# Kernel tuning notes

Measured on AMD Instinct MI355X. Metric: run time of the kernel, lower is better.

## Reference

```python
import jax, jax.numpy as jnp
import numpy as np

N_LAYERS = 4
BN_EPS = 1e-5


def setup_inputs() -> dict:
    key = jax.random.key(0)
    ks = jax.random.split(key, 10)
    N, E, F, H = 50000, 600000, 128, 128
    x = jax.random.normal(ks[0], (N, F), dtype=jnp.float32)
    edge_index = jax.random.randint(ks[1], (2, E), 0, N, dtype=jnp.int64)
    s = 0.05  # small init to keep deep ReLU stack numerically tame
    return {
        "x": x,
        "edge_index": edge_index,
        # stacked params for the 4 GINConv MLPs (num_features == hidden)
        "conv_w1": jax.random.normal(ks[2], (N_LAYERS, F, H), dtype=jnp.float32) * s,
        "conv_b1": jnp.zeros((N_LAYERS, H), dtype=jnp.float32),
        "conv_gamma": jnp.ones((N_LAYERS, H), dtype=jnp.float32),
        "conv_beta": jnp.zeros((N_LAYERS, H), dtype=jnp.float32),
        "conv_w2": jax.random.normal(ks[3], (N_LAYERS, H, H), dtype=jnp.float32) * s,
        "conv_b2": jnp.zeros((N_LAYERS, H), dtype=jnp.float32),
        "fc1_w": jax.random.normal(ks[4], (H, H), dtype=jnp.float32) * s,
        "fc1_b": jnp.zeros((H,), dtype=jnp.float32),
        "fc2_w": jax.random.normal(ks[5], (H, 1), dtype=jnp.float32) * s,
        "fc2_b": jnp.zeros((1,), dtype=jnp.float32),
    }


def _batchnorm(h, gamma, beta):
    # training-mode BatchNorm1d: batch stats over the node axis, biased variance
    mean = jnp.mean(h, axis=0, keepdims=True)
    var = jnp.mean(jnp.square(h - mean), axis=0, keepdims=True)
    return (h - mean) * jax.lax.rsqrt(var + BN_EPS) * gamma + beta


def _gin_layer(x, src, dst, w1, b1, gamma, beta, w2, b2):
    n = x.shape[0]
    # GIN sum aggregation with eps=0: (1+eps)*x_i + sum_{j->i} x_j
    agg = x + jax.ops.segment_sum(x[src], dst, num_segments=n)
    h = jax.nn.relu(agg @ w1 + b1)
    h = _batchnorm(h, gamma, beta)
    return jax.nn.relu(h @ w2 + b2)


def reference(x, edge_index, conv_w1, conv_b1, conv_gamma, conv_beta,
              conv_w2, conv_b2, fc1_w, fc1_b, fc2_w, fc2_b):
    src, dst = edge_index[0], edge_index[1]
    h = x
    for l in range(N_LAYERS):
        h = _gin_layer(h, src, dst, conv_w1[l], conv_b1[l], conv_gamma[l],
                       conv_beta[l], conv_w2[l], conv_b2[l])
    h = jax.nn.relu(h @ fc1_w + fc1_b)
    return h @ fc2_w + fc2_b  # [N, 1]
```

## Files before the change

kernel.cpp:

```cpp
#include <hip/hip_runtime.h>

constexpr int FEAT = 128;

typedef __attribute__((ext_vector_type(8))) _Float16 f16x8;
typedef __attribute__((ext_vector_type(4))) float f32x4;

__device__ inline unsigned int halfpair(float a, float b) {
  unsigned short ua = __builtin_bit_cast(unsigned short, (_Float16)a);
  unsigned short ub = __builtin_bit_cast(unsigned short, (_Float16)b);
  return (unsigned int)ua | ((unsigned int)ub << 16);
}
__device__ inline unsigned short halfr(float a) {
  return __builtin_bit_cast(unsigned short, (_Float16)a);
}
__device__ inline float2 halfup(unsigned int u) {
  _Float16 lo = __builtin_bit_cast(_Float16, (unsigned short)(u & 0xffffu));
  _Float16 hi = __builtin_bit_cast(_Float16, (unsigned short)(u >> 16));
  return make_float2((float)lo, (float)hi);
}

__device__ __host__ inline int kperm(int k) {
  return ((k >> 5) << 5) + (((k >> 2) & 3) << 3) + (((k >> 4) & 1) << 2) + (k & 3);
}


__global__ void count_kernel(const int* __restrict__ dst, int* __restrict__ deg, int E) {
  int e = blockIdx.x * blockDim.x + threadIdx.x;
  if (e < E) atomicAdd(&deg[dst[e]], 1);
}

__global__ __launch_bounds__(1024) void scan_kernel(const int* __restrict__ in,
                                                    int* __restrict__ out,
                                                    int* __restrict__ out2, int n) {
  __shared__ int wsum[16];
  __shared__ int carry;
  int tid = threadIdx.x;
  if (tid == 0) carry = 0;
  __syncthreads();
  int lane = tid & 63, wid = tid >> 6;
  for (int base = 0; base < n; base += 1024) {
    int i = base + tid;
    int v = (i < n) ? in[i] : 0;
    int s = v;
#pragma unroll
    for (int off = 1; off < 64; off <<= 1) {
      int t = __shfl_up(s, off);
      if (lane >= off) s += t;
    }
    if (lane == 63) wsum[wid] = s;
    __syncthreads();
    if (tid < 16) {
      int ws2 = wsum[tid];
#pragma unroll
      for (int off = 1; off < 16; off <<= 1) {
        int t = __shfl_up(ws2, off, 16);
        if ((tid & 15) >= off) ws2 += t;
      }
      wsum[tid] = ws2;
    }
    __syncthreads();
    int excl = carry + (wid ? wsum[wid - 1] : 0) + (s - v);
    if (i < n) { out[i] = excl; out2[i] = excl; }
    __syncthreads();
    if (tid == 0) carry += wsum[15];
    __syncthreads();
  }
}

__global__ void fill_kernel(const int* __restrict__ src, const int* __restrict__ dst,
                            int* __restrict__ cursor, int* __restrict__ col, int E) {
  int e = blockIdx.x * blockDim.x + threadIdx.x;
  if (e < E) {
    int p = atomicAdd(&cursor[dst[e]], 1);
    col[p] = src[e];
  }
}


__global__ void convert_kernel(const float* __restrict__ x, unsigned short* __restrict__ xb,
                               int n4) {
  int idx = blockIdx.x * blockDim.x + threadIdx.x;
  if (idx >= n4) return;
  float4 v = ((const float4*)x)[idx];
  uint2 o;
  o.x = halfpair(v.x, v.y);
  o.y = halfpair(v.z, v.w);
  ((uint2*)xb)[idx] = o;
}


__global__ void wconv_kernel(const float* __restrict__ w1, const float* __restrict__ fc1w,
                             unsigned short* __restrict__ dst) {
  int idx = blockIdx.x * blockDim.x + threadIdx.x;
  if (idx >= 5 * FEAT * FEAT) return;
  int m = idx >> 14;
  int r = idx & (FEAT * FEAT - 1);
  int k = r >> 7, n = r & 127;
  float v = (m < 4) ? w1[idx] : fc1w[r];
  int p = kperm(k);
  int slot = p >> 3, e = p & 7;
  dst[m * FEAT * FEAT + n * FEAT + ((slot ^ (n & 7)) << 3) + e] = halfr(v);
}


__global__ void agg_kernel(const unsigned short* __restrict__ x, const int* __restrict__ rowptr,
                           const int* __restrict__ col, unsigned short* __restrict__ agg, int N) {
  int gid = blockIdx.x * blockDim.x + threadIdx.x;
  int wid = gid >> 6;
  int lane = threadIdx.x & 63;
  int node = wid * 4 + (lane >> 4);
  if (node >= N) return;
  int ln = lane & 15;
  const uint4* xr = (const uint4*)x;
  uint4 s = xr[(size_t)node * 16 + ln];
  float2 t0 = halfup(s.x), t1 = halfup(s.y), t2 = halfup(s.z), t3 = halfup(s.w);
  float a0 = t0.x, a1 = t0.y, a2 = t1.x, a3 = t1.y;
  float a4 = t2.x, a5 = t2.y, a6 = t3.x, a7 = t3.y;
  float b0 = 0.f, b1 = 0.f, b2 = 0.f, b3 = 0.f;
  float b4 = 0.f, b5 = 0.f, b6 = 0.f, b7 = 0.f;
  int e0 = rowptr[node], e1 = rowptr[node + 1];
  int e = e0;
  for (; e + 1 < e1; e += 2) {
    int c0 = col[e], c1 = col[e + 1];
    uint4 v = xr[(size_t)c0 * 16 + ln];
    uint4 u = xr[(size_t)c1 * 16 + ln];
    float2 v0 = halfup(v.x), v1 = halfup(v.y), v2 = halfup(v.z), v3 = halfup(v.w);
    float2 u0 = halfup(u.x), u1 = halfup(u.y), u2 = halfup(u.z), u3 = halfup(u.w);
    a0 += v0.x; a1 += v0.y; a2 += v1.x; a3 += v1.y;
    a4 += v2.x; a5 += v2.y; a6 += v3.x; a7 += v3.y;
    b0 += u0.x; b1 += u0.y; b2 += u1.x; b3 += u1.y;
    b4 += u2.x; b5 += u2.y; b6 += u3.x; b7 += u3.y;
  }
  if (e < e1) {
    uint4 v = xr[(size_t)col[e] * 16 + ln];
    float2 v0 = halfup(v.x), v1 = halfup(v.y), v2 = halfup(v.z), v3 = halfup(v.w);
    a0 += v0.x; a1 += v0.y; a2 += v1.x; a3 += v1.y;
    a4 += v2.x; a5 += v2.y; a6 += v3.x; a7 += v3.y;
  }
  a0 += b0; a1 += b1; a2 += b2; a3 += b3;
  a4 += b4; a5 += b5; a6 += b6; a7 += b7;
  uint4 o;
  o.x = halfpair(a0, a1);
  o.y = halfpair(a2, a3);
  o.z = halfpair(a4, a5);
  o.w = halfpair(a6, a7);
  ((uint4*)agg)[(size_t)node * 16 + ln] = o;
}


__global__ __launch_bounds__(256) void gemm_kernel(
    const unsigned short* __restrict__ A, const unsigned short* __restrict__ Wimg,
    const float* __restrict__ bias, unsigned short* __restrict__ C,
    float* __restrict__ pS, float* __restrict__ pQ, int N, int doStats) {
  __shared__ unsigned short Al[FEAT * FEAT];
  __shared__ unsigned short Wl[FEAT * FEAT];
  __shared__ float ls[FEAT], lq[FEAT];

  int tx = threadIdx.x;
  int row0 = blockIdx.x * FEAT;
  if (tx < FEAT) { ls[tx] = 0.f; lq[tx] = 0.f; }

#pragma unroll
  for (int i = 0; i < 8; i++) {
    int idx = tx + i * 256;
    ((uint4*)Wl)[idx] = ((const uint4*)Wimg)[idx];
  }
#pragma unroll
  for (int i = 0; i < 16; i++) {
    int idx = tx + i * 256;
    int r = idx >> 5;
    int c = idx & 31;
    uint2 v = make_uint2(0u, 0u);
    if (row0 + r < N) v = ((const uint2*)(A + (size_t)(row0 + r) * FEAT))[c];
    int k0 = c << 2;
    int p0 = ((k0 >> 5) << 5) + (((k0 >> 2) & 3) << 3) + (((k0 >> 4) & 1) << 2);
    int slot = p0 >> 3, half4 = (p0 >> 2) & 1;
    *(uint2*)&Al[r * FEAT + ((slot ^ (r & 7)) << 3) + (half4 << 2)] = v;
  }
  __syncthreads();

  int w = tx >> 6;
  int l = tx & 63;
  int llo = l & 15, lhi = l >> 4;
  int wr = (w >> 1) * 64, wc = (w & 1) * 64;

  f32x4 acc[4][4];
#pragma unroll
  for (int mi = 0; mi < 4; mi++)
#pragma unroll
    for (int nj = 0; nj < 4; nj++) acc[mi][nj] = (f32x4)(0.f);

#pragma unroll
  for (int s = 0; s < 4; s++) {
    f16x8 af[4], wf[4];
#pragma unroll
    for (int mi = 0; mi < 4; mi++) {
      int row = wr + mi * 16 + llo;
      int base = row * FEAT + ((((s << 2) + lhi) ^ (row & 7)) << 3);
      af[mi] = *(const f16x8*)&Al[base];
    }
#pragma unroll
    for (int nj = 0; nj < 4; nj++) {
      int n = wc + nj * 16 + llo;
      int base = n * FEAT + ((((s << 2) + lhi) ^ (n & 7)) << 3);
      wf[nj] = *(const f16x8*)&Wl[base];
    }
#pragma unroll
    for (int mi = 0; mi < 4; mi++)
#pragma unroll
      for (int nj = 0; nj < 4; nj++)
        acc[mi][nj] = __builtin_amdgcn_mfma_f32_16x16x32_f16(wf[nj], af[mi], acc[mi][nj], 0, 0, 0);
  }

#pragma unroll
  for (int nj = 0; nj < 4; nj++) {
    int colb = wc + nj * 16 + lhi * 4;
    float4 bb = *(const float4*)&bias[colb];
    float ps[4] = {0.f, 0.f, 0.f, 0.f}, pq[4] = {0.f, 0.f, 0.f, 0.f};
#pragma unroll
    for (int mi = 0; mi < 4; mi++) {
      int row = row0 + wr + mi * 16 + llo;
      f32x4 v = acc[mi][nj];
      float v0 = fmaxf(v[0] + bb.x, 0.f);
      float v1 = fmaxf(v[1] + bb.y, 0.f);
      float v2 = fmaxf(v[2] + bb.z, 0.f);
      float v3 = fmaxf(v[3] + bb.w, 0.f);
      if (row < N) {
        *(uint2*)&C[(size_t)row * FEAT + colb] = make_uint2(halfpair(v0, v1), halfpair(v2, v3));
        ps[0] += v0; ps[1] += v1; ps[2] += v2; ps[3] += v3;
        pq[0] += v0 * v0; pq[1] += v1 * v1; pq[2] += v2 * v2; pq[3] += v3 * v3;
      }
    }
    if (doStats) {
#pragma unroll
      for (int r = 0; r < 4; r++) {
        float s2 = ps[r], q2 = pq[r];
#pragma unroll
        for (int off = 1; off < 16; off <<= 1) {
          s2 += __shfl_xor(s2, off);
          q2 += __shfl_xor(q2, off);
        }
        if (llo == 0) {
          atomicAdd(&ls[colb + r], s2);
          atomicAdd(&lq[colb + r], q2);
        }
      }
    }
  }
  if (doStats) {
    __syncthreads();
    if (tx < FEAT) {
      pS[(size_t)blockIdx.x * FEAT + tx] = ls[tx];
      pQ[(size_t)blockIdx.x * FEAT + tx] = lq[tx];
    }
  }
}


__global__ __launch_bounds__(64) void stats_kernel(
    const float* __restrict__ pS, const float* __restrict__ pQ, int nblk,
    const float* __restrict__ gamma, const float* __restrict__ beta,
    float* __restrict__ scf, float* __restrict__ shf, int N) {
  int c = blockIdx.x;
  int ln = threadIdx.x;
  float s = 0.f, q = 0.f;
  for (int b = ln; b < nblk; b += 64) {
    s += pS[(size_t)b * FEAT + c];
    q += pQ[(size_t)b * FEAT + c];
  }
#pragma unroll
  for (int off = 32; off; off >>= 1) {
    s += __shfl_xor(s, off);
    q += __shfl_xor(q, off);
  }
  if (ln == 0) {
    float invN = 1.0f / (float)N;
    float mean = s * invN;
    float var = q * invN - mean * mean;
    float rstd = rsqrtf(var + 1e-5f);
    float scale = gamma[c] * rstd;
    scf[c] = scale;
    shf[c] = beta[c] - mean * scale;
  }
}


__global__ __launch_bounds__(128) void fold2_kernel(
    const float* __restrict__ scf, const float* __restrict__ shf,
    const float* __restrict__ w2, const float* __restrict__ b2,
    unsigned short* __restrict__ w2f, float* __restrict__ b2f) {
  __shared__ float red[FEAT];
  int c = blockIdx.x;
  int k = threadIdx.x;
  float wv = w2[k * FEAT + c];
  int p = kperm(k);
  int slot = p >> 3, e = p & 7;
  w2f[c * FEAT + ((slot ^ (c & 7)) << 3) + e] = halfr(scf[k] * wv);
  red[k] = shf[k] * wv;
  __syncthreads();
#pragma unroll
  for (int off = 64; off > 0; off >>= 1) {
    if (k < off) red[k] += red[k + off];
    __syncthreads();
  }
  if (k == 0) b2f[c] = b2[c] + red[0];
}


__global__ void fc2_kernel(const unsigned short* __restrict__ h, const float* __restrict__ w,
                           const float* __restrict__ b, float* __restrict__ out, int N) {
  int gid = blockIdx.x * blockDim.x + threadIdx.x;
  int node = gid >> 6;
  if (node >= N) return;
  int lane = threadIdx.x & 63;
  float2 hv = halfup(((const unsigned int*)h)[(size_t)node * 64 + lane]);
  float2 wv = ((const float2*)w)[lane];
  float s = hv.x * wv.x + hv.y * wv.y;
#pragma unroll
  for (int off = 32; off; off >>= 1) s += __shfl_xor(s, off);
  if (lane == 0) out[node] = s + b[0];
}


extern "C" void kernel_launch(void* const* d_in, const int* in_sizes, int n_in,
                              void* d_out, int out_size, void* d_ws, size_t ws_size,
                              hipStream_t stream) {
  const float* x     = (const float*)d_in[0];
  const int*   ei    = (const int*)d_in[1];
  const float* w1    = (const float*)d_in[2];
  const float* b1    = (const float*)d_in[3];
  const float* gamma = (const float*)d_in[4];
  const float* beta  = (const float*)d_in[5];
  const float* w2    = (const float*)d_in[6];
  const float* b2    = (const float*)d_in[7];
  const float* fc1w  = (const float*)d_in[8];
  const float* fc1b  = (const float*)d_in[9];
  const float* fc2w  = (const float*)d_in[10];
  const float* fc2b  = (const float*)d_in[11];
  float* out = (float*)d_out;

  int N = in_sizes[0] / FEAT;
  int E = in_sizes[1] / 2;
  const int* srcI = ei;
  const int* dstI = ei + E;

  int gemmBlocks = (N + FEAT - 1) / FEAT;

  size_t Nf = (size_t)N * FEAT;
  unsigned short* H = (unsigned short*)d_ws;
  unsigned short* G = H + Nf;
  unsigned short* wimg = G + Nf;
  unsigned short* w2f = wimg + 5 * FEAT * FEAT;
  float* b2f = (float*)(w2f + FEAT * FEAT);
  float* scf = b2f + FEAT;
  float* shf = scf + FEAT;
  float* pS = shf + FEAT;
  float* pQ = pS + (size_t)gemmBlocks * FEAT;
  int* deg = (int*)(pQ + (size_t)gemmBlocks * FEAT);
  int* rowptr = deg + (N + 1);
  int* cursor = rowptr + (N + 1);
  int* col = cursor + (N + 1);

  hipMemsetAsync(deg, 0, (N + 1) * sizeof(int), stream);
  count_kernel<<<(E + 255) / 256, 256, 0, stream>>>(dstI, deg, E);
  scan_kernel<<<1, 1024, 0, stream>>>(deg, rowptr, cursor, N + 1);
  fill_kernel<<<(E + 255) / 256, 256, 0, stream>>>(srcI, dstI, cursor, col, E);

  int n4 = (int)(Nf / 4);
  convert_kernel<<<(n4 + 255) / 256, 256, 0, stream>>>(x, H, n4);
  wconv_kernel<<<(5 * FEAT * FEAT + 255) / 256, 256, 0, stream>>>(w1, fc1w, wimg);

  int aggBlocks = (int)((((size_t)(N + 3) / 4) * 64 + 255) / 256);
  int fc2Blocks = (int)(((size_t)N * 64 + 255) / 256);

  for (int l = 0; l < 4; l++) {
    agg_kernel<<<aggBlocks, 256, 0, stream>>>(H, rowptr, col, G, N);
    gemm_kernel<<<gemmBlocks, 256, 0, stream>>>(G, wimg + (size_t)l * FEAT * FEAT,
                                                b1 + (size_t)l * FEAT, G, pS, pQ, N, 1);
    stats_kernel<<<FEAT, 64, 0, stream>>>(pS, pQ, gemmBlocks, gamma + (size_t)l * FEAT,
                                          beta + (size_t)l * FEAT, scf, shf, N);
    fold2_kernel<<<FEAT, FEAT, 0, stream>>>(scf, shf, w2 + (size_t)l * FEAT * FEAT,
                                            b2 + (size_t)l * FEAT, w2f, b2f);
    gemm_kernel<<<gemmBlocks, 256, 0, stream>>>(G, w2f, b2f, H, nullptr, nullptr, N, 0);
  }

  gemm_kernel<<<gemmBlocks, 256, 0, stream>>>(H, wimg + (size_t)4 * FEAT * FEAT, fc1b, G,
                                              nullptr, nullptr, N, 0);
  fc2_kernel<<<fc2Blocks, 256, 0, stream>>>(G, fc2w, fc2b, out, N);
}
```

Baseline: 475.3 us.

## Parallelize CSR prefix scan across blocks and unroll neighbor gather by four

Replaces the single-block serial-loop scan over node degrees with a three-pass multi-block scan (block sums, scan of block sums, per-block prefix with int4 vector loads and stores). This removes a long serialized kernel that used one workgroup for about 50k entries. The aggregation loop is also unrolled from two to four neighbors per iteration so more gathers are in flight. The scan of block sums handles at most 64 blocks in one wave, which caps the node count. Workspace offsets are padded to 4-int alignment for the vector accesses.

```diff
diff --git a/kernel.cpp b/kernel.cpp
--- a/kernel.cpp
+++ b/kernel.cpp
@@ -29,41 +29,78 @@
   if (e < E) atomicAdd(&deg[dst[e]], 1);
 }
 
-__global__ __launch_bounds__(1024) void scan_kernel(const int* __restrict__ in,
+__global__ __launch_bounds__(256) void scan1_kernel(const int* __restrict__ in,
+                                                    int* __restrict__ bsum, int n) {
+  int base = blockIdx.x * 1024 + threadIdx.x * 4;
+  int s = 0;
+  if (base + 3 < n) {
+    int4 v = *(const int4*)(in + base);
+    s = v.x + v.y + v.z + v.w;
+  } else {
+#pragma unroll
+    for (int j = 0; j < 4; j++)
+      if (base + j < n) s += in[base + j];
+  }
+#pragma unroll
+  for (int off = 1; off < 64; off <<= 1) s += __shfl_xor(s, off);
+  __shared__ int ws[4];
+  int lane = threadIdx.x & 63, wid = threadIdx.x >> 6;
+  if (lane == 0) ws[wid] = s;
+  __syncthreads();
+  if (threadIdx.x == 0) bsum[blockIdx.x] = ws[0] + ws[1] + ws[2] + ws[3];
+}
+
+__global__ __launch_bounds__(64) void scan2_kernel(int* __restrict__ bsum, int nb) {
+  int t = threadIdx.x;
+  int v = (t < nb) ? bsum[t] : 0;
+  int s = v;
+#pragma unroll
+  for (int off = 1; off < 64; off <<= 1) {
+    int u = __shfl_up(s, off);
+    if (t >= off) s += u;
+  }
+  if (t < nb) bsum[t] = s - v;
+}
+
+__global__ __launch_bounds__(256) void scan3_kernel(const int* __restrict__ in,
+                                                    const int* __restrict__ boff,
                                                     int* __restrict__ out,
                                                     int* __restrict__ out2, int n) {
-  __shared__ int wsum[16];
-  __shared__ int carry;
-  int tid = threadIdx.x;
-  if (tid == 0) carry = 0;
+  int t = threadIdx.x;
+  int base = blockIdx.x * 1024 + t * 4;
+  int v0 = 0, v1 = 0, v2 = 0, v3 = 0;
+  if (base + 3 < n) {
+    int4 v = *(const int4*)(in + base);
+    v0 = v.x; v1 = v.y; v2 = v.z; v3 = v.w;
+  } else {
+    if (base + 0 < n) v0 = in[base + 0];
+    if (base + 1 < n) v1 = in[base + 1];
+    if (base + 2 < n) v2 = in[base + 2];
+  }
+  int ts = v0 + v1 + v2 + v3;
+  int s = ts;
+  int lane = t & 63, wid = t >> 6;
+#pragma unroll
+  for (int off = 1; off < 64; off <<= 1) {
+    int u = __shfl_up(s, off);
+    if (lane >= off) s += u;
+  }
+  __shared__ int ws[4];
+  if (lane == 63) ws[wid] = s;
   __syncthreads();
-  int lane = tid & 63, wid = tid >> 6;
-  for (int base = 0; base < n; base += 1024) {
-    int i = base + tid;
-    int v = (i < n) ? in[i] : 0;
-    int s = v;
-#pragma unroll
-    for (int off = 1; off < 64; off <<= 1) {
-      int t = __shfl_up(s, off);
-      if (lane >= off) s += t;
-    }
-    if (lane == 63) wsum[wid] = s;
-    __syncthreads();
-    if (tid < 16) {
-      int ws2 = wsum[tid];
-#pragma unroll
-      for (int off = 1; off < 16; off <<= 1) {
-        int t = __shfl_up(ws2, off, 16);
-        if ((tid & 15) >= off) ws2 += t;
-      }
-      wsum[tid] = ws2;
-    }
-    __syncthreads();
-    int excl = carry + (wid ? wsum[wid - 1] : 0) + (s - v);
-    if (i < n) { out[i] = excl; out2[i] = excl; }
-    __syncthreads();
-    if (tid == 0) carry += wsum[15];
-    __syncthreads();
+  int cross = 0;
+#pragma unroll
+  for (int i = 0; i < 4; i++)
+    if (i < wid) cross += ws[i];
+  int excl = boff[blockIdx.x] + cross + (s - ts);
+  int o0 = excl, o1 = o0 + v0, o2 = o1 + v1, o3 = o2 + v2;
+  if (base + 3 < n) {
+    *(int4*)(out + base) = make_int4(o0, o1, o2, o3);
+    *(int4*)(out2 + base) = make_int4(o0, o1, o2, o3);
+  } else {
+    if (base + 0 < n) { out[base + 0] = o0; out2[base + 0] = o0; }
+    if (base + 1 < n) { out[base + 1] = o1; out2[base + 1] = o1; }
+    if (base + 2 < n) { out[base + 2] = o2; out2[base + 2] = o2; }
   }
 }
 
@@ -120,22 +157,37 @@
   float b4 = 0.f, b5 = 0.f, b6 = 0.f, b7 = 0.f;
   int e0 = rowptr[node], e1 = rowptr[node + 1];
   int e = e0;
-  for (; e + 1 < e1; e += 2) {
-    int c0 = col[e], c1 = col[e + 1];
+  for (; e + 3 < e1; e += 4) {
+    int c0 = col[e], c1 = col[e + 1], c2 = col[e + 2], c3 = col[e + 3];
     uint4 v = xr[(size_t)c0 * 16 + ln];
     uint4 u = xr[(size_t)c1 * 16 + ln];
-    float2 v0 = halfup(v.x), v1 = halfup(v.y), v2 = halfup(v.z), v3 = halfup(v.w);
-    float2 u0 = halfup(u.x), u1 = halfup(u.y), u2 = halfup(u.z), u3 = halfup(u.w);
-    a0 += v0.x; a1 += v0.y; a2 += v1.x; a3 += v1.y;
-    a4 += v2.x; a5 += v2.y; a6 += v3.x; a7 += v3.y;
-    b0 += u0.x; b1 += u0.y; b2 += u1.x; b3 += u1.y;
-    b4 += u2.x; b5 += u2.y; b6 += u3.x; b7 += u3.y;
-  }
-  if (e < e1) {
+    uint4 w = xr[(size_t)c2 * 16 + ln];
+    uint4 z = xr[(size_t)c3 * 16 + ln];
+    float2 f;
+    f = halfup(v.x); a0 += f.x; a1 += f.y;
+    f = halfup(v.y); a2 += f.x; a3 += f.y;
+    f = halfup(v.z); a4 += f.x; a5 += f.y;
+    f = halfup(v.w); a6 += f.x; a7 += f.y;
+    f = halfup(u.x); b0 += f.x; b1 += f.y;
+    f = halfup(u.y); b2 += f.x; b3 += f.y;
+    f = halfup(u.z); b4 += f.x; b5 += f.y;
+    f = halfup(u.w); b6 += f.x; b7 += f.y;
+    f = halfup(w.x); a0 += f.x; a1 += f.y;
+    f = halfup(w.y); a2 += f.x; a3 += f.y;
+    f = halfup(w.z); a4 += f.x; a5 += f.y;
+    f = halfup(w.w); a6 += f.x; a7 += f.y;
+    f = halfup(z.x); b0 += f.x; b1 += f.y;
+    f = halfup(z.y); b2 += f.x; b3 += f.y;
+    f = halfup(z.z); b4 += f.x; b5 += f.y;
+    f = halfup(z.w); b6 += f.x; b7 += f.y;
+  }
+  for (; e < e1; e++) {
     uint4 v = xr[(size_t)col[e] * 16 + ln];
-    float2 v0 = halfup(v.x), v1 = halfup(v.y), v2 = halfup(v.z), v3 = halfup(v.w);
-    a0 += v0.x; a1 += v0.y; a2 += v1.x; a3 += v1.y;
-    a4 += v2.x; a5 += v2.y; a6 += v3.x; a7 += v3.y;
+    float2 f;
+    f = halfup(v.x); a0 += f.x; a1 += f.y;
+    f = halfup(v.y); a2 += f.x; a3 += f.y;
+    f = halfup(v.z); a4 += f.x; a5 += f.y;
+    f = halfup(v.w); a6 += f.x; a7 += f.y;
   }
   a0 += b0; a1 += b1; a2 += b2; a3 += b3;
   a4 += b4; a5 += b5; a6 += b6; a7 += b7;
@@ -345,6 +397,8 @@
   const int* dstI = ei + E;
 
   int gemmBlocks = (N + FEAT - 1) / FEAT;
+  int n = N + 1;
+  int nb = (n + 1023) / 1024;
 
   size_t Nf = (size_t)N * FEAT;
   unsigned short* H = (unsigned short*)d_ws;
@@ -357,13 +411,16 @@
   float* pS = shf + FEAT;
   float* pQ = pS + (size_t)gemmBlocks * FEAT;
   int* deg = (int*)(pQ + (size_t)gemmBlocks * FEAT);
-  int* rowptr = deg + (N + 1);
-  int* cursor = rowptr + (N + 1);
-  int* col = cursor + (N + 1);
-
-  hipMemsetAsync(deg, 0, (N + 1) * sizeof(int), stream);
+  int* rowptr = deg + ((n + 3) & ~3);
+  int* cursor = rowptr + ((n + 3) & ~3);
+  int* bsum = cursor + ((n + 3) & ~3);
+  int* col = bsum + 64;
+
+  hipMemsetAsync(deg, 0, n * sizeof(int), stream);
   count_kernel<<<(E + 255) / 256, 256, 0, stream>>>(dstI, deg, E);
-  scan_kernel<<<1, 1024, 0, stream>>>(deg, rowptr, cursor, N + 1);
+  scan1_kernel<<<nb, 256, 0, stream>>>(deg, bsum, n);
+  scan2_kernel<<<1, 64, 0, stream>>>(bsum, nb);
+  scan3_kernel<<<nb, 256, 0, stream>>>(deg, bsum, rowptr, cursor, n);
   fill_kernel<<<(E + 255) / 256, 256, 0, stream>>>(srcI, dstI, cursor, col, E);
 
   int n4 = (int)(Nf / 4);
```

Measured after the change: 425.2 us. 10.5% less time.
